# Kernel optimization log

Hardware: AMD Instinct MI355X
Metric: run time of the kernel (lower is better)

The kernel has to match this reference:

```python
import jax, jax.numpy as jnp
import numpy as np

TERNARY_THRESHOLD = 0.001

def _ternarize(t):
    # {-1, 0, 1} with dead zone of width 2*TERNARY_THRESHOLD
    return jnp.where(t > TERNARY_THRESHOLD, 1.0,
                     jnp.where(t < -TERNARY_THRESHOLD, -1.0, 0.0)).astype(t.dtype)

def setup_inputs() -> dict:
    key = jax.random.key(0)
    k_x, k_w1, k_b1, k_w2, k_b2 = jax.random.split(key, 5)
    B, D_IN, D_H, D_OUT = 65536, 784, 320, 10
    x = jax.random.normal(k_x, (B, D_IN), dtype=jnp.float32)
    # nn.Linear layout: weight [out_features, in_features]
    w1 = jax.random.normal(k_w1, (D_H, D_IN), dtype=jnp.float32) * 0.05
    b1 = jax.random.normal(k_b1, (D_H,), dtype=jnp.float32) * 0.05
    w2 = jax.random.normal(k_w2, (D_OUT, D_H), dtype=jnp.float32) * 0.05
    b2 = jax.random.normal(k_b2, (D_OUT,), dtype=jnp.float32) * 0.05
    return {"x": x, "w1": w1, "b1": b1, "w2": w2, "b2": b2}

def reference(x, w1, b1, w2, b2):
    x = x.reshape(-1, 784)
    # TernaryLinear: clamp weight to [-1,1], ternarize, then F.linear
    q1 = _ternarize(jnp.clip(w1, -1.0, 1.0))
    h = x @ q1.T + b1                       # [B, 320]
    h = _ternarize(h)                       # ternary activation
    q2 = _ternarize(jnp.clip(w2, -1.0, 1.0))
    logits = h @ q2.T + b2                  # [B, 10]
    return jax.nn.log_softmax(logits, axis=1)
```

## Files before the change

kernel.cpp:

```cpp
#include <hip/hip_runtime.h>
#include <stdint.h>


#define TERN_TH 0.001f

using bf16x8 = __attribute__((ext_vector_type(8))) short;
using f32x4  = __attribute__((ext_vector_type(4))) float;

__device__ __forceinline__ unsigned short f2bf(float f) {
    unsigned u = __float_as_uint(f);
    u = (u + 0x7FFFu + ((u >> 16) & 1u)) >> 16;
    return (unsigned short)u;
}
__device__ __forceinline__ float bf2f(unsigned short h) {
    return __uint_as_float(((unsigned)h) << 16);
}
__device__ __forceinline__ float ternf(float w) {
    return (w > TERN_TH) ? 1.0f : ((w < -TERN_TH) ? -1.0f : 0.0f);
}

__device__ __forceinline__ void split8(float4 a, float4 b, bf16x8& hi, bf16x8& lo) {
    float v[8] = {a.x, a.y, a.z, a.w, b.x, b.y, b.z, b.w};
    bf16x8 h, l;
#pragma unroll
    for (int i = 0; i < 8; ++i) {
        unsigned short hh = f2bf(v[i]);
        h[i] = (short)hh;
        l[i] = (short)f2bf(v[i] - bf2f(hh));
    }
    hi = h; lo = l;
}

#define Q1F_ELEMS (25 * 20 * 4 * 16 * 8)
__global__ void prep_q1(const float* __restrict__ w1, unsigned short* __restrict__ q1f) {
    int idx = blockIdx.x * 256 + threadIdx.x;
    if (idx >= Q1F_ELEMS) return;
    int kk   = idx & 7;
    int col  = (idx >> 3) & 15;
    int quad = (idx >> 7) & 3;
    int t    = idx >> 9;
    int nt   = t % 20;
    int c    = t / 20;
    int k = c * 32 + quad * 8 + kk;
    int j = nt * 16 + col;
    float v = (k < 784) ? ternf(w1[j * 784 + k]) : 0.0f;
    q1f[idx] = f2bf(v);
}

#define LDS_H   0
#define LDS_Q2  41984
#define LDS_TOTAL 52480

__global__ __launch_bounds__(256, 2) void mlp_main(
    const float* __restrict__ x, const unsigned short* __restrict__ q1f,
    const float* __restrict__ b1, const float* __restrict__ w2,
    const float* __restrict__ b2, float* __restrict__ out) {

    __shared__ __attribute__((aligned(16))) unsigned char smem[LDS_TOTAL];
    unsigned short* sm16 = (unsigned short*)smem;

    const int tid  = threadIdx.x;
    const int lane = tid & 63;
    const int wave = tid >> 6;
    const int quad = lane >> 4;
    const int l15  = lane & 15;
    const int blk  = blockIdx.x;

    f32x4 acc[2][20];
#pragma unroll
    for (int mt = 0; mt < 2; ++mt)
#pragma unroll
        for (int nt = 0; nt < 20; ++nt) {
            f32x4 z = {0.f, 0.f, 0.f, 0.f};
            acc[mt][nt] = z;
        }

    const int rowbase = blk * 128 + wave * 32;
    const float* xr0 = x + (size_t)(rowbase + l15) * 784;
    const float* xr1 = x + (size_t)(rowbase + 16 + l15) * 784;
    const unsigned short* bq1 = q1f + (size_t)quad * 128 + (size_t)l15 * 8;

    for (int c = 0; c < 25; ++c) {
        int kq  = c * 32 + quad * 8;
        int kqs = (kq < 784) ? kq : 0;

        bf16x8 ahi0, alo0, ahi1, alo1;
        {
            const float4* p0 = (const float4*)(xr0 + kqs);
            const float4* p1 = (const float4*)(xr1 + kqs);
            float4 a0 = p0[0], b0 = p0[1];
            float4 a1 = p1[0], b1_ = p1[1];
            split8(a0, b0, ahi0, alo0);
            split8(a1, b1_, ahi1, alo1);
        }

        const unsigned short* bp = bq1 + (size_t)c * 10240;
#pragma unroll
        for (int nt = 0; nt < 20; ++nt) {
            bf16x8 bq = *(const bf16x8*)(bp + (size_t)nt * 512);
            acc[0][nt] = __builtin_amdgcn_mfma_f32_16x16x32_bf16(ahi0, bq, acc[0][nt], 0, 0, 0);
            acc[0][nt] = __builtin_amdgcn_mfma_f32_16x16x32_bf16(alo0, bq, acc[0][nt], 0, 0, 0);
            acc[1][nt] = __builtin_amdgcn_mfma_f32_16x16x32_bf16(ahi1, bq, acc[1][nt], 0, 0, 0);
            acc[1][nt] = __builtin_amdgcn_mfma_f32_16x16x32_bf16(alo1, bq, acc[1][nt], 0, 0, 0);
        }
    }

    for (int idx = tid; idx < 16 * 328; idx += 256) {
        int o = idx / 328, j = idx % 328;
        float v = (o < 10 && j < 320) ? ternf(w2[o * 320 + j]) : 0.0f;
        sm16[(LDS_Q2 >> 1) + idx] = f2bf(v);
    }
    float b1v[20];
#pragma unroll
    for (int nt = 0; nt < 20; ++nt) b1v[nt] = b1[nt * 16 + l15];
    float b2v = (l15 < 10) ? b2[l15] : 0.0f;

    for (int pass = 0; pass < 2; ++pass) {
        __syncthreads();
        if ((wave >> 1) == pass) {
#pragma unroll
            for (int mt = 0; mt < 2; ++mt)
#pragma unroll
                for (int nt = 0; nt < 20; ++nt)
#pragma unroll
                    for (int i = 0; i < 4; ++i) {
                        float hv = acc[mt][nt][i] + b1v[nt];
                        int row = (wave & 1) * 32 + mt * 16 + quad * 4 + i;
                        int col = nt * 16 + l15;
                        sm16[(LDS_H >> 1) + row * 328 + col] = f2bf(ternf(hv));
                    }
        }
        __syncthreads();
        f32x4 acc2 = {0.f, 0.f, 0.f, 0.f};
#pragma unroll
        for (int kc = 0; kc < 10; ++kc) {
            bf16x8 a = *(const bf16x8*)(smem + LDS_H + (wave * 16 + l15) * 656 + kc * 64 + quad * 16);
            bf16x8 b = *(const bf16x8*)(smem + LDS_Q2 + l15 * 656 + kc * 64 + quad * 16);
            acc2 = __builtin_amdgcn_mfma_f32_16x16x32_bf16(a, b, acc2, 0, 0, 0);
        }
#pragma unroll
        for (int i = 0; i < 4; ++i) {
            float l  = acc2[i] + b2v;
            float lm = (l15 < 10) ? l : -3.4e38f;
#pragma unroll
            for (int s = 8; s >= 1; s >>= 1) lm = fmaxf(lm, __shfl_xor(lm, s, 64));
            float e  = (l15 < 10) ? expf(l - lm) : 0.0f;
            float ss = e;
#pragma unroll
            for (int s = 8; s >= 1; s >>= 1) ss += __shfl_xor(ss, s, 64);
            float ov = (l - lm) - logf(ss);
            if (l15 < 10) {
                int grow = blk * 128 + pass * 64 + wave * 16 + quad * 4 + i;
                out[(size_t)grow * 10 + l15] = ov;
            }
        }
    }
}

extern "C" void kernel_launch(void* const* d_in, const int* in_sizes, int n_in,
                              void* d_out, int out_size, void* d_ws, size_t ws_size,
                              hipStream_t stream) {
    const float* x  = (const float*)d_in[0];
    const float* w1 = (const float*)d_in[1];
    const float* b1 = (const float*)d_in[2];
    const float* w2 = (const float*)d_in[3];
    const float* b2 = (const float*)d_in[4];
    unsigned short* q1f = (unsigned short*)d_ws;

    prep_q1<<<(Q1F_ELEMS + 255) / 256, 256, 0, stream>>>(w1, q1f);
    mlp_main<<<512, 256, 0, stream>>>(x, q1f, b1, w2, b2, (float*)d_out);
}
```

Measured before the change: 406.9 us.

## Stage Q1 weight chunks in double-buffered LDS and prefetch next x chunk

The Q1 weight tile for each K-chunk is now loaded cooperatively by the whole block into registers, stored to one of two LDS buffers, and read from LDS by all waves. Before, each wave loaded it separately from global memory. The next chunk's weights and x values are prefetched into registers while the current chunk's MFMAs run, to hide global load latency. This adds a __syncthreads per chunk and more register pressure (br, xn) on a kernel already holding 160 accumulator floats per thread.

```diff
diff --git a/kernel.cpp b/kernel.cpp
--- a/kernel.cpp
+++ b/kernel.cpp
@@ -47,6 +47,8 @@
     q1f[idx] = f2bf(v);
 }
 
+#define BCHUNK_U4 1280
+#define LDS_BBUF(i) ((i) * 20480)
 #define LDS_H   0
 #define LDS_Q2  41984
 #define LDS_TOTAL 52480
@@ -78,33 +80,60 @@
     const int rowbase = blk * 128 + wave * 32;
     const float* xr0 = x + (size_t)(rowbase + l15) * 784;
     const float* xr1 = x + (size_t)(rowbase + 16 + l15) * 784;
-    const unsigned short* bq1 = q1f + (size_t)quad * 128 + (size_t)l15 * 8;
+    const uint4* bsrc = (const uint4*)q1f;
+
+    uint4  br[5];
+    float4 xc[4];
+    float4 xn[4];
+
+    {
+#pragma unroll
+        for (int i = 0; i < 5; ++i) br[i] = bsrc[tid + i * 256];
+        const float4* p0 = (const float4*)(xr0);
+        const float4* p1 = (const float4*)(xr1);
+        xc[0] = p0[quad * 2]; xc[1] = p0[quad * 2 + 1];
+        xc[2] = p1[quad * 2]; xc[3] = p1[quad * 2 + 1];
+    }
 
     for (int c = 0; c < 25; ++c) {
-        int kq  = c * 32 + quad * 8;
-        int kqs = (kq < 784) ? kq : 0;
-
-        bf16x8 ahi0, alo0, ahi1, alo1;
         {
+            uint4* dst = (uint4*)(smem + LDS_BBUF(c & 1));
+#pragma unroll
+            for (int i = 0; i < 5; ++i) dst[tid + i * 256] = br[i];
+        }
+        __syncthreads();
+
+        if (c < 24) {
+            int cn = c + 1;
+            const uint4* src = bsrc + (size_t)cn * BCHUNK_U4;
+#pragma unroll
+            for (int i = 0; i < 5; ++i) br[i] = src[tid + i * 256];
+            int kq  = cn * 32 + quad * 8;
+            int kqs = (kq < 784) ? kq : 0;
             const float4* p0 = (const float4*)(xr0 + kqs);
             const float4* p1 = (const float4*)(xr1 + kqs);
-            float4 a0 = p0[0], b0 = p0[1];
-            float4 a1 = p1[0], b1_ = p1[1];
-            split8(a0, b0, ahi0, alo0);
-            split8(a1, b1_, ahi1, alo1);
-        }
-
-        const unsigned short* bp = bq1 + (size_t)c * 10240;
+            xn[0] = p0[0]; xn[1] = p0[1];
+            xn[2] = p1[0]; xn[3] = p1[1];
+        }
+
+        bf16x8 ahi0, alo0, ahi1, alo1;
+        split8(xc[0], xc[1], ahi0, alo0);
+        split8(xc[2], xc[3], ahi1, alo1);
+
+        const unsigned char* bp = smem + LDS_BBUF(c & 1) + quad * 256 + l15 * 16;
 #pragma unroll
         for (int nt = 0; nt < 20; ++nt) {
-            bf16x8 bq = *(const bf16x8*)(bp + (size_t)nt * 512);
+            bf16x8 bq = *(const bf16x8*)(bp + nt * 1024);
             acc[0][nt] = __builtin_amdgcn_mfma_f32_16x16x32_bf16(ahi0, bq, acc[0][nt], 0, 0, 0);
             acc[0][nt] = __builtin_amdgcn_mfma_f32_16x16x32_bf16(alo0, bq, acc[0][nt], 0, 0, 0);
             acc[1][nt] = __builtin_amdgcn_mfma_f32_16x16x32_bf16(ahi1, bq, acc[1][nt], 0, 0, 0);
             acc[1][nt] = __builtin_amdgcn_mfma_f32_16x16x32_bf16(alo1, bq, acc[1][nt], 0, 0, 0);
         }
-    }
-
+#pragma unroll
+        for (int i = 0; i < 4; ++i) xc[i] = xn[i];
+    }
+
+    __syncthreads();
     for (int idx = tid; idx < 16 * 328; idx += 256) {
         int o = idx / 328, j = idx % 328;
         float v = (o < 10 && j < 320) ? ternf(w2[o * 320 + j]) : 0.0f;
```

Measured after the change: 369.9 us. 9.1% less time.
